# Kernel optimization log

Hardware: AMD Instinct MI355X
Metric: run time of the kernel (lower is better)

## Reference

```python
import jax, jax.numpy as jnp
import numpy as np

IMAGE_SIZE = 224
COV_HP = 1.0
SIGMA = 1.0
STEPS = 2
CUTOFF = 20.0
IMP_LO, IMP_HI = 0.5, 2.0
REL_W = 0.5
EPS = 1e-6

# Projection matrices for front/top/left views (buffer Js in the module)
JS = jnp.array([[[1, 0, 0], [0, 1, 0]],
                [[1, 0, 0], [0, 0, 1]],
                [[0, 0, 1], [0, 1, 0]]], dtype=jnp.float32)


def _blur(d, sigma):
    # d: [B,H,W]; separable Gaussian blur, 'same' padding
    r = max(1, int(3 * sigma))
    x = jnp.arange(-r, r + 1, dtype=jnp.float32)
    k = jnp.exp(-(x * x) / (2.0 * sigma * sigma))
    k = k / k.sum()
    d4 = d[:, None]  # [B,1,H,W]
    kh = k.reshape(1, 1, -1, 1)
    kw = k.reshape(1, 1, 1, -1)
    d4 = jax.lax.conv_general_dilated(d4, kh, (1, 1), [(r, r), (0, 0)],
                                      dimension_numbers=('NCHW', 'OIHW', 'NCHW'))
    d4 = jax.lax.conv_general_dilated(d4, kw, (1, 1), [(0, 0), (r, r)],
                                      dimension_numbers=('NCHW', 'OIHW', 'NCHW'))
    return d4[:, 0]


def _fill_depth_map(d, sigma, steps):
    # fill_depth_map is not defined in the source; implemented as iterative
    # Gaussian-blur hole filling (empty pixels take blurred neighborhood).
    for _ in range(steps):
        b = _blur(d, sigma)
        d = jnp.where(d > 1e-6, d, b)
    return d


def _forward(position, cov3d, opacity, importance):
    B, N, _ = position.shape
    H = W = IMAGE_SIZE
    Hh, Wh = H // 2, W // 2
    yy, xx = jnp.meshgrid(jnp.arange(Hh), jnp.arange(Wh), indexing='ij')
    grid = jnp.stack([xx, yy], axis=-1).astype(jnp.float32)  # [Hh,Wh,2]
    imp = jnp.clip(jnp.broadcast_to(importance[:, :N], (B, N)), IMP_LO, IMP_HI)
    imp = imp[:, :, None, None]
    eye3 = jnp.eye(3, dtype=cov3d.dtype)
    eye2 = jnp.eye(2, dtype=cov3d.dtype)
    maps = []
    for v in range(3):  # fixed small view loop, as in the source
        J = JS[v]  # [2,3]
        # NOTE: source mutates cov3d across the view loop; replicate that
        cov3d = (cov3d + jnp.swapaxes(cov3d, -1, -2)) * 0.5
        cov3d = cov3d + EPS * eye3
        nrm = jnp.linalg.norm(cov3d, axis=(-1, -2), keepdims=True)
        cov3d = cov3d / (nrm + EPS) * COV_HP
        cinv = jnp.linalg.inv(cov3d)                               # [B,N,3,3]
        cov2d_inv = jnp.einsum('ij,bnjk,lk->bnil', J, cinv, J)     # J C^-1 J^T
        cov2d_inv = cov2d_inv + eye2 * (EPS * 1e-4)
        proj = jnp.einsum('bnk,jk->bnj', position, J)              # [B,N,2]
        mn = proj.min(axis=1, keepdims=True)
        mx = proj.max(axis=1, keepdims=True)
        rng = mx - mn + 1e-6
        mn = mn - 0.5 * rng
        mx = mx + 0.5 * rng
        rng = mx - mn + 1e-6
        xy = jnp.clip((proj - mn) / rng * (Wh - 1), 0.0, Wh - 1)
        delta = grid[None, None] - xy[:, :, None, None, :]         # [B,N,Hh,Wh,2]
        mask_h = jnp.linalg.norm(delta, axis=-1) < CUTOFF
        mask = jnp.repeat(jnp.repeat(mask_h, 2, axis=2), 2, axis=3)
        exph = -jnp.einsum('bnhwj,bnjk,bnhwk->bnhw', delta, cov2d_inv, delta)
        exp_full = jax.image.resize(exph, (B, N, H, W), method='bilinear')
        exp_full = jnp.clip(exp_full, -20.0, 0.0)
        w = opacity[:, :, None, None] * imp * jnp.exp(exp_full)
        w = jnp.where(mask, w, 0.0)
        wmin = w.min(axis=1, keepdims=True)
        wmax = w.max(axis=1, keepdims=True)
        nw = (w - wmin) / (wmax - wmin + EPS) * REL_W + w / (w.sum(axis=1, keepdims=True) + EPS)
        dm = nw.sum(axis=1)  # [B,H,W]
        maps.append(_fill_depth_map(dm, SIGMA, STEPS))
    d = jnp.stack(maps, axis=1)  # [B,3,H,W], already 224x224 so resize is a no-op
    d = (d - d.mean()) / (jnp.std(d, ddof=1) + EPS)
    return d


def setup_inputs() -> dict:
    key = jax.random.key(0)
    k1, k2, k3 = jax.random.split(key, 3)
    B, N, MAXG = 1, 512, 1000
    return {
        'position': jax.random.normal(k1, (B, N, 3), dtype=jnp.float32),
        'cov3d': jax.random.normal(k2, (B, N, 3, 3), dtype=jnp.float32),
        'opacity': jax.random.uniform(k3, (B, N), dtype=jnp.float32),
        'importance': jnp.ones((1, MAXG), dtype=jnp.float32),
    }


def reference(position, cov3d, opacity, importance):
    return _forward(position, cov3d, opacity, importance)
```

## Files before the change

kernel.cpp:

```cpp
#include <hip/hip_runtime.h>
#include <math.h>


#define NBLOCKS 588u
#define NARR 32
#define FLAG_IDX (NARR * 32)
#define KSPLIT 4
#define QOFF 12544
#define MNOFF 602112
#define MXOFF 1204224

__device__ __forceinline__ float g_ld(const float* p) {
    return __hip_atomic_load(p, __ATOMIC_RELAXED, __HIP_MEMORY_SCOPE_AGENT);
}
__device__ __forceinline__ void g_st(float* p, float v) {
    __hip_atomic_store(p, v, __ATOMIC_RELAXED, __HIP_MEMORY_SCOPE_AGENT);
}

__device__ __forceinline__ void grid_barrier(unsigned* cnts, int arrIdx, bool poller) {
    __syncthreads();
    if (threadIdx.x == 0) {
        asm volatile("s_waitcnt vmcnt(0)" ::: "memory");
        __hip_atomic_fetch_add(&cnts[arrIdx * 32], 1u,
                               __ATOMIC_RELAXED, __HIP_MEMORY_SCOPE_AGENT);
        unsigned* flagp = &cnts[FLAG_IDX];
        if (poller) {
            for (;;) {
                unsigned s = 0;
                #pragma unroll
                for (int i = 0; i < NARR; ++i)
                    s += __hip_atomic_load(&cnts[i * 32],
                                           __ATOMIC_RELAXED, __HIP_MEMORY_SCOPE_AGENT);
                if (s == NBLOCKS) break;
                __builtin_amdgcn_s_sleep(2);
            }
            asm volatile("" ::: "memory");
            __hip_atomic_store(flagp, 1u, __ATOMIC_RELAXED, __HIP_MEMORY_SCOPE_AGENT);
        } else {
            while (__hip_atomic_load(flagp, __ATOMIC_RELAXED,
                                     __HIP_MEMORY_SCOPE_AGENT) == 0u)
                __builtin_amdgcn_s_sleep(2);
        }
    }
    __syncthreads();
}

__device__ __forceinline__ float wave_min(float v) {
    #pragma unroll
    for (int o = 32; o >= 1; o >>= 1) v = fminf(v, __shfl_xor(v, o));
    return v;
}

__global__ __launch_bounds__(512) void setup_kernel(
    const float* __restrict__ position, const float* __restrict__ cov3d,
    const float* __restrict__ opacity, const float* __restrict__ importance,
    float4* __restrict__ abc, float2* __restrict__ gxy,
    unsigned* __restrict__ cnts) {
    __shared__ float red[8 * 6];
    const int v = blockIdx.x;
    const int tid = threadIdx.x;
    const int lane = tid & 63, wave = tid >> 6;

    if (v == 0) {
        for (int i = tid; i <= FLAG_IDX; i += 512) cnts[i] = 0;
    }

    const int n = tid;
    const float p0 = position[n * 3 + 0];
    const float p1 = position[n * 3 + 1];
    const float p2 = position[n * 3 + 2];
    const float opimp = opacity[n] * fminf(fmaxf(importance[n], 0.5f), 2.0f);

    {
        float vals[6] = {p0, -p0, p1, -p1, p2, -p2};
        #pragma unroll
        for (int k = 0; k < 6; ++k) {
            float r = wave_min(vals[k]);
            if (lane == 0) red[wave * 6 + k] = r;
        }
    }
    __syncthreads();
    float mn6[6];
    #pragma unroll
    for (int k = 0; k < 6; ++k) {
        float r = red[k];
        #pragma unroll
        for (int w = 1; w < 8; ++w) r = fminf(r, red[w * 6 + k]);
        mn6[k] = r;
    }
    const float pmn[3] = {mn6[0], mn6[2], mn6[4]};
    const float pmx[3] = {-mn6[1], -mn6[3], -mn6[5]};

    float c00 = cov3d[n * 9 + 0], c01 = cov3d[n * 9 + 1], c02 = cov3d[n * 9 + 2];
    float c10 = cov3d[n * 9 + 3], c11 = cov3d[n * 9 + 4], c12 = cov3d[n * 9 + 5];
    float c20 = cov3d[n * 9 + 6], c21 = cov3d[n * 9 + 7], c22 = cov3d[n * 9 + 8];
    for (int vv = 0; vv <= v; ++vv) {
        float s01 = 0.5f * (c01 + c10);
        float s02 = 0.5f * (c02 + c20);
        float s12 = 0.5f * (c12 + c21);
        float s00 = c00 + 1e-6f;
        float s11 = c11 + 1e-6f;
        float s22 = c22 + 1e-6f;
        float nrm = sqrtf(s00 * s00 + s11 * s11 + s22 * s22 +
                          2.0f * (s01 * s01 + s02 * s02 + s12 * s12));
        float inv = 1.0f / (nrm + 1e-6f);
        c00 = s00 * inv; c11 = s11 * inv; c22 = s22 * inv;
        c01 = s01 * inv; c10 = c01; c02 = s02 * inv; c20 = c02;
        c12 = s12 * inv; c21 = c12;
    }
    float cof00 = c11 * c22 - c12 * c12;
    float cof01 = c02 * c12 - c01 * c22;
    float cof02 = c01 * c12 - c02 * c11;
    float det = c00 * cof00 + c01 * cof01 + c02 * cof02;
    float idet = 1.0f / det;
    float i00 = cof00 * idet;
    float i01 = cof01 * idet;
    float i02 = cof02 * idet;
    float i11 = (c00 * c22 - c02 * c02) * idet;
    float i12 = (c02 * c01 - c00 * c12) * idet;
    float i22 = (c00 * c11 - c01 * c01) * idet;

    float Aa, Ab, Ac, prx, pry;
    int ix, iy;
    if (v == 0)      { Aa = i00; Ab = i01; Ac = i11; prx = p0; pry = p1; ix = 0; iy = 1; }
    else if (v == 1) { Aa = i00; Ab = i02; Ac = i22; prx = p0; pry = p2; ix = 0; iy = 2; }
    else             { Aa = i22; Ab = i12; Ac = i11; prx = p2; pry = p1; ix = 2; iy = 1; }
    Aa += 1e-10f;
    Ac += 1e-10f;

    float mnx = pmn[ix], mxx = pmx[ix], mny = pmn[iy], mxy = pmx[iy];
    float rngx = mxx - mnx + 1e-6f;
    float mnx2 = mnx - 0.5f * rngx;
    float mxx2 = mxx + 0.5f * rngx;
    rngx = mxx2 - mnx2 + 1e-6f;
    float rngy = mxy - mny + 1e-6f;
    float mny2 = mny - 0.5f * rngy;
    float mxy2 = mxy + 0.5f * rngy;
    rngy = mxy2 - mny2 + 1e-6f;
    float gx = fminf(fmaxf((prx - mnx2) / rngx * 111.0f, 0.0f), 111.0f);
    float gy = fminf(fmaxf((pry - mny2) / rngy * 111.0f, 0.0f), 111.0f);

    abc[v * 512 + n] = make_float4(Aa, 2.0f * Ab, Ac, opimp);
    gxy[v * 512 + n] = make_float2(gx, gy);
}

__global__ __launch_bounds__(512) void splat_part_kernel(
    const float4* __restrict__ abc, const float2* __restrict__ gxy,
    float* __restrict__ part) {
    __shared__ float4 lsA[512];
    __shared__ float2 lsB[512];
    __shared__ int wcnt[8];
    __shared__ float4 pS[7][64], pMn[7][64], pMx[7][64];
    const int v  = blockIdx.z >> 2;
    const int kk = blockIdx.z & 3;
    const int tx0 = blockIdx.x * 16, ty0 = blockIdx.y * 16;
    const int tid = threadIdx.x;
    const int lane = tid & 63, wave = tid >> 6;

    const float4 a4 = abc[v * 512 + tid];
    const float2 g2 = gxy[v * 512 + tid];

    unsigned long long m;
    bool pass;
    {
        const float bx0 = (float)(tx0 >> 1), bx1 = (float)((tx0 + 15) >> 1);
        const float by0 = (float)(ty0 >> 1), by1 = (float)((ty0 + 15) >> 1);
        float dx = fmaxf(fmaxf(bx0 - g2.x, g2.x - bx1), 0.0f);
        float dy = fmaxf(fmaxf(by0 - g2.y, g2.y - by1), 0.0f);
        pass = (dx * dx + dy * dy) < 400.01f;
        m = __ballot(pass);
        if (lane == 0) wcnt[wave] = __popcll(m);
    }
    __syncthreads();
    int base = 0, lentot = 0;
    #pragma unroll
    for (int w = 0; w < 8; ++w) {
        int c = wcnt[w];
        if (w < wave) base += c;
        lentot += c;
    }
    if (pass) {
        int slot = base + __popcll(m & ((1ull << lane) - 1ull));
        lsA[slot] = a4;
        lsB[slot] = g2;
    }
    __syncthreads();
    const int len = lentot;

    const int qx = lane & 7, qy = lane >> 3;
    const int xh = (tx0 >> 1) + qx;
    const int yh = (ty0 >> 1) + qy;

    const int npad = (len + 63) & ~63;
    if (tid < npad - len) {
        lsA[len + tid] = make_float4(1.0f, 0.0f, 1.0f, 0.0f);
        lsB[len + tid] = make_float2(1e9f, 1e9f);
    }
    __syncthreads();

    float exA[2], eyA[2], VxA[2], VyA[2];
    #pragma unroll
    for (int p = 0; p < 2; ++p) {
        int xlo = xh - 1 + p; int xhi = min(xlo + 1, 111); xlo = max(xlo, 0);
        float wlo = p ? 0.75f : 0.25f, whi = 1.0f - wlo;
        exA[p] = wlo * (float)xlo + whi * (float)xhi;
        VxA[p] = wlo * whi * (float)(xhi - xlo) * (float)(xhi - xlo);
        int ylo = yh - 1 + p; int yhi2 = min(ylo + 1, 111); ylo = max(ylo, 0);
        eyA[p] = wlo * (float)ylo + whi * (float)yhi2;
        VyA[p] = wlo * whi * (float)(yhi2 - ylo) * (float)(yhi2 - ylo);
    }
    const float fxh = (float)xh, fyh = (float)yh;

    const int chunk = npad >> 5;
    const int cbeg = ((kk << 3) + wave) * chunk, cend = cbeg + chunk;

    float S00 = 0.f, S01 = 0.f, S10 = 0.f, S11 = 0.f;
    float mn00 = INFINITY, mn01 = INFINITY, mn10 = INFINITY, mn11 = INFINITY;
    float mx00 = -INFINITY, mx01 = -INFINITY, mx10 = -INFINITY, mx11 = -INFINITY;

    for (int i = cbeg; i < cend; i += 2) {
        float4 gA0 = lsA[i], gA1 = lsA[i + 1];
        float2 gB0 = lsB[i], gB1 = lsB[i + 1];
        #pragma unroll
        for (int u = 0; u < 2; ++u) {
            const float4 gA = u ? gA1 : gA0;
            const float2 gB = u ? gB1 : gB0;
            const float a = gA.x, b2 = gA.y, c = gA.z, op = gA.w;
            const float xx = gB.x, yy = gB.y;
            const float dxh = fxh - xx, dyh = fyh - yy;
            const bool inside = dxh * dxh + dyh * dyh < 400.0f;
            const float dx0 = exA[0] - xx, dx1 = exA[1] - xx;
            const float dy0 = eyA[0] - yy, dy1 = eyA[1] - yy;
            const float adx0 = a * dx0, adx1 = a * dx1;
            const float bdy0 = b2 * dy0, bdy1 = b2 * dy1;
            const float cdy0 = c * dy0 * dy0, cdy1 = c * dy1 * dy1;
            const float ax0 = a * VxA[0], ax1 = a * VxA[1];
            const float cy0 = c * VyA[0], cy1 = c * VyA[1];
            #pragma unroll
            for (int py = 0; py < 2; ++py) {
                const float bdyp = py ? bdy1 : bdy0;
                const float cdyp = py ? cdy1 : cdy0;
                const float cyp  = py ? cy1 : cy0;
                #pragma unroll
                for (int px = 0; px < 2; ++px) {
                    const float dxp  = px ? dx1 : dx0;
                    const float adxp = px ? adx1 : adx0;
                    const float axp  = px ? ax1 : ax0;
                    float q = dxp * (adxp + bdyp) + cdyp;
                    float bil = -((q + axp) + cyp);
                    bil = fminf(fmaxf(bil, -20.0f), 0.0f);
                    bil = inside ? bil : -1e9f;
                    float w = op * __expf(bil);
                    if (py == 0 && px == 0) { S00 += w; mn00 = fminf(mn00, w); mx00 = fmaxf(mx00, w); }
                    if (py == 0 && px == 1) { S01 += w; mn01 = fminf(mn01, w); mx01 = fmaxf(mx01, w); }
                    if (py == 1 && px == 0) { S10 += w; mn10 = fminf(mn10, w); mx10 = fmaxf(mx10, w); }
                    if (py == 1 && px == 1) { S11 += w; mn11 = fminf(mn11, w); mx11 = fmaxf(mx11, w); }
                }
            }
        }
    }
    if (wave > 0) {
        pS[wave - 1][lane]  = make_float4(S00, S01, S10, S11);
        pMn[wave - 1][lane] = make_float4(mn00, mn01, mn10, mn11);
        pMx[wave - 1][lane] = make_float4(mx00, mx01, mx10, mx11);
    }
    __syncthreads();
    if (wave == 0) {
        #pragma unroll
        for (int w = 0; w < 7; ++w) {
            float4 s = pS[w][lane], mnw = pMn[w][lane], mxw = pMx[w][lane];
            S00 += s.x; S01 += s.y; S10 += s.z; S11 += s.w;
            mn00 = fminf(mn00, mnw.x); mn01 = fminf(mn01, mnw.y);
            mn10 = fminf(mn10, mnw.z); mn11 = fminf(mn11, mnw.w);
            mx00 = fmaxf(mx00, mxw.x); mx01 = fmaxf(mx01, mxw.y);
            mx10 = fmaxf(mx10, mxw.z); mx11 = fmaxf(mx11, mxw.w);
        }
        if (len < 512) {
            mn00 = fminf(mn00, 0.f); mn01 = fminf(mn01, 0.f);
            mn10 = fminf(mn10, 0.f); mn11 = fminf(mn11, 0.f);
            mx00 = fmaxf(mx00, 0.f); mx01 = fmaxf(mx01, 0.f);
            mx10 = fmaxf(mx10, 0.f); mx11 = fmaxf(mx11, 0.f);
        }
        const int qidx = (kk * 3 + v) * QOFF + yh * 112 + xh;
        ((float4*)(part))[qidx]          = make_float4(S00, S01, S10, S11);
        ((float4*)(part + MNOFF))[qidx]  = make_float4(mn00, mn01, mn10, mn11);
        ((float4*)(part + MXOFF))[qidx]  = make_float4(mx00, mx01, mx10, mx11);
    }
}

__global__ __launch_bounds__(256, 3) void blur_norm_kernel(
    const float* __restrict__ part, float* __restrict__ out,
    float2* __restrict__ partials, unsigned* __restrict__ cnts) {
    __shared__ float A[28 * 29];
    __shared__ float T[28 * 29];
    __shared__ float r1[4], r2[4];
    __shared__ double s1[256], s2[256];
    const int v = blockIdx.z;
    const int tx0 = blockIdx.x * 16, ty0 = blockIdx.y * 16;
    const int tid = threadIdx.x;
    const int lane = tid & 63, wave = tid >> 6;
    const int bid = (v * 14 + blockIdx.y) * 14 + blockIdx.x;
    const float kw[7] = {0.00443305f, 0.05400558f, 0.24203623f, 0.39905030f,
                         0.24203623f, 0.05400558f, 0.00443305f};

    for (int idx = tid; idx < 28 * 28; idx += 256) {
        int rr = idx / 28, c = idx % 28;
        int gyy = ty0 - 6 + rr, gxx = tx0 - 6 + c;
        float val = 0.0f;
        if (gyy >= 0 && gyy < 224 && gxx >= 0 && gxx < 224) {
            const int qb = (gyy >> 1) * 112 + (gxx >> 1);
            const int comp = ((gyy & 1) << 1) | (gxx & 1);
            float S = 0.0f, mn = INFINITY, mx = -INFINITY;
            #pragma unroll
            for (int k = 0; k < KSPLIT; ++k) {
                const int fi = ((k * 3 + v) * QOFF + qb) * 4 + comp;
                S += part[fi];
                mn = fminf(mn, part[MNOFF + fi]);
                mx = fmaxf(mx, part[MXOFF + fi]);
            }
            val = 0.5f * (S - 512.0f * mn) / (mx - mn + 1e-6f) + S / (S + 1e-6f);
        }
        A[rr * 29 + c] = val;
    }
    __syncthreads();
    for (int idx = tid; idx < 22 * 28; idx += 256) {
        int rr = 3 + idx / 28, c = idx % 28;
        float s = 0.0f;
        #pragma unroll
        for (int i = 0; i < 7; ++i) s += kw[i] * A[(rr - 3 + i) * 29 + c];
        T[rr * 29 + c] = s;
    }
    __syncthreads();
    for (int idx = tid; idx < 22 * 22; idx += 256) {
        int rr = 3 + idx / 22, c = 3 + idx % 22;
        int gyy = ty0 - 6 + rr, gxx = tx0 - 6 + c;
        float s = 0.0f;
        #pragma unroll
        for (int j = 0; j < 7; ++j) s += kw[j] * T[rr * 29 + c - 3 + j];
        float ctr = A[rr * 29 + c];
        float d1 = ctr > 1e-6f ? ctr : s;
        if (gyy < 0 || gyy > 223 || gxx < 0 || gxx > 223) d1 = 0.0f;
        A[rr * 29 + c] = d1;
    }
    __syncthreads();
    for (int idx = tid; idx < 16 * 22; idx += 256) {
        int rr = 6 + idx / 22, c = 3 + idx % 22;
        float s = 0.0f;
        #pragma unroll
        for (int i = 0; i < 7; ++i) s += kw[i] * A[(rr - 3 + i) * 29 + c];
        T[rr * 29 + c] = s;
    }
    __syncthreads();
    const int rr2 = 6 + (tid >> 4), cc2 = 6 + (tid & 15);
    float d2;
    {
        float s = 0.0f;
        #pragma unroll
        for (int j = 0; j < 7; ++j) s += kw[j] * T[rr2 * 29 + cc2 - 3 + j];
        float ctr = A[rr2 * 29 + cc2];
        d2 = ctr > 1e-6f ? ctr : s;
    }
    float ls1 = d2, ls2 = d2 * d2;
    #pragma unroll
    for (int o = 32; o >= 1; o >>= 1) {
        ls1 += __shfl_xor(ls1, o);
        ls2 += __shfl_xor(ls2, o);
    }
    if (lane == 0) { r1[wave] = ls1; r2[wave] = ls2; }
    __syncthreads();
    if (tid == 0) {
        float a = r1[0] + r1[1] + r1[2] + r1[3];
        float b = r2[0] + r2[1] + r2[2] + r2[3];
        float* pb = (float*)&partials[bid];
        g_st(pb + 0, a);
        g_st(pb + 1, b);
    }

    grid_barrier(cnts, bid & (NARR - 1), bid == 0);

    double a = 0.0, b = 0.0;
    const float* pb = (const float*)partials;
    for (int i = tid; i < 588; i += 256) {
        a += (double)g_ld(pb + 2 * i);
        b += (double)g_ld(pb + 2 * i + 1);
    }
    s1[tid] = a; s2[tid] = b;
    __syncthreads();
    for (int s = 128; s >= 1; s >>= 1) {
        if (tid < s) { s1[tid] += s1[tid + s]; s2[tid] += s2[tid + s]; }
        __syncthreads();
    }
    const double M = 150528.0;
    double mean = s1[0] / M;
    double var = (s2[0] - M * mean * mean) / (M - 1.0);
    double sd = sqrt(var > 0.0 ? var : 0.0);
    const float fmean = (float)mean;
    const float finv = 1.0f / ((float)sd + 1e-6f);
    out[(v * 224 + ty0 + (tid >> 4)) * 224 + tx0 + (tid & 15)] =
        (d2 - fmean) * finv;
}

extern "C" void kernel_launch(void* const* d_in, const int* in_sizes, int n_in,
                              void* d_out, int out_size, void* d_ws, size_t ws_size,
                              hipStream_t stream) {
    const float* position   = (const float*)d_in[0];
    const float* cov3d      = (const float*)d_in[1];
    const float* opacity    = (const float*)d_in[2];
    const float* importance = (const float*)d_in[3];
    float* out = (float*)d_out;

    float* part      = (float*)d_ws;
    float2* partials = (float2*)((float*)d_ws + 1806336);
    unsigned* cnts   = (unsigned*)((float*)d_ws + 1806336 + 1176);
    float4* abc      = (float4*)((float*)d_ws + 1808640);
    float2* gxy      = (float2*)((float*)d_ws + 1808640 + 6144);

    hipLaunchKernelGGL(setup_kernel, dim3(3), dim3(512), 0, stream,
                       position, cov3d, opacity, importance, abc, gxy, cnts);
    hipLaunchKernelGGL(splat_part_kernel, dim3(14, 14, 3 * KSPLIT), dim3(512), 0,
                       stream, abc, gxy, part);
    hipLaunchKernelGGL(blur_norm_kernel, dim3(14, 14, 3), dim3(256), 0, stream,
                       part, out, partials, cnts);
}
```

Before: 97.02 us.

## Halve splat K-split, vectorize quad loads, and centralize final stats reduction

```diff
diff --git a/kernel.cpp b/kernel.cpp
--- a/kernel.cpp
+++ b/kernel.cpp
@@ -5,44 +5,17 @@
 #define NBLOCKS 588u
 #define NARR 32
 #define FLAG_IDX (NARR * 32)
-#define KSPLIT 4
+#define STAT_IDX (FLAG_IDX + 32)
+#define KSPLIT 2
 #define QOFF 12544
-#define MNOFF 602112
-#define MXOFF 1204224
+#define MNOFF 301056
+#define MXOFF 602112
 
 __device__ __forceinline__ float g_ld(const float* p) {
     return __hip_atomic_load(p, __ATOMIC_RELAXED, __HIP_MEMORY_SCOPE_AGENT);
 }
 __device__ __forceinline__ void g_st(float* p, float v) {
     __hip_atomic_store(p, v, __ATOMIC_RELAXED, __HIP_MEMORY_SCOPE_AGENT);
-}
-
-__device__ __forceinline__ void grid_barrier(unsigned* cnts, int arrIdx, bool poller) {
-    __syncthreads();
-    if (threadIdx.x == 0) {
-        asm volatile("s_waitcnt vmcnt(0)" ::: "memory");
-        __hip_atomic_fetch_add(&cnts[arrIdx * 32], 1u,
-                               __ATOMIC_RELAXED, __HIP_MEMORY_SCOPE_AGENT);
-        unsigned* flagp = &cnts[FLAG_IDX];
-        if (poller) {
-            for (;;) {
-                unsigned s = 0;
-                #pragma unroll
-                for (int i = 0; i < NARR; ++i)
-                    s += __hip_atomic_load(&cnts[i * 32],
-                                           __ATOMIC_RELAXED, __HIP_MEMORY_SCOPE_AGENT);
-                if (s == NBLOCKS) break;
-                __builtin_amdgcn_s_sleep(2);
-            }
-            asm volatile("" ::: "memory");
-            __hip_atomic_store(flagp, 1u, __ATOMIC_RELAXED, __HIP_MEMORY_SCOPE_AGENT);
-        } else {
-            while (__hip_atomic_load(flagp, __ATOMIC_RELAXED,
-                                     __HIP_MEMORY_SCOPE_AGENT) == 0u)
-                __builtin_amdgcn_s_sleep(2);
-        }
-    }
-    __syncthreads();
 }
 
 __device__ __forceinline__ float wave_min(float v) {
@@ -62,7 +35,7 @@
     const int lane = tid & 63, wave = tid >> 6;
 
     if (v == 0) {
-        for (int i = tid; i <= FLAG_IDX; i += 512) cnts[i] = 0;
+        for (int i = tid; i < STAT_IDX + 32; i += 512) cnts[i] = 0;
     }
 
     const int n = tid;
@@ -151,8 +124,8 @@
     __shared__ float2 lsB[512];
     __shared__ int wcnt[8];
     __shared__ float4 pS[7][64], pMn[7][64], pMx[7][64];
-    const int v  = blockIdx.z >> 2;
-    const int kk = blockIdx.z & 3;
+    const int v  = blockIdx.z >> 1;
+    const int kk = blockIdx.z & 1;
     const int tx0 = blockIdx.x * 16, ty0 = blockIdx.y * 16;
     const int tid = threadIdx.x;
     const int lane = tid & 63, wave = tid >> 6;
@@ -211,7 +184,7 @@
     }
     const float fxh = (float)xh, fyh = (float)yh;
 
-    const int chunk = npad >> 5;
+    const int chunk = npad >> 4;
     const int cbeg = ((kk << 3) + wave) * chunk, cend = cbeg + chunk;
 
     float S00 = 0.f, S01 = 0.f, S10 = 0.f, S11 = 0.f;
@@ -295,6 +268,7 @@
     __shared__ float T[28 * 29];
     __shared__ float r1[4], r2[4];
     __shared__ double s1[256], s2[256];
+    __shared__ float statLds[2];
     const int v = blockIdx.z;
     const int tx0 = blockIdx.x * 16, ty0 = blockIdx.y * 16;
     const int tid = threadIdx.x;
@@ -303,24 +277,37 @@
     const float kw[7] = {0.00443305f, 0.05400558f, 0.24203623f, 0.39905030f,
                          0.24203623f, 0.05400558f, 0.00443305f};
 
-    for (int idx = tid; idx < 28 * 28; idx += 256) {
-        int rr = idx / 28, c = idx % 28;
-        int gyy = ty0 - 6 + rr, gxx = tx0 - 6 + c;
-        float val = 0.0f;
-        if (gyy >= 0 && gyy < 224 && gxx >= 0 && gxx < 224) {
-            const int qb = (gyy >> 1) * 112 + (gxx >> 1);
-            const int comp = ((gyy & 1) << 1) | (gxx & 1);
-            float S = 0.0f, mn = INFINITY, mx = -INFINITY;
+    {
+        const float4* Sp  = (const float4*)part;
+        const float4* Mnp = (const float4*)(part + MNOFF);
+        const float4* Mxp = (const float4*)(part + MXOFF);
+        const int qy0 = (ty0 - 6) >> 1, qx0 = (tx0 - 6) >> 1;
+        if (tid < 196) {
+            const int qr = tid / 14, qc = tid % 14;
+            const int qgy = qy0 + qr, qgx = qx0 + qc;
+            float dmv[4] = {0.0f, 0.0f, 0.0f, 0.0f};
+            if (qgy >= 0 && qgy < 112 && qgx >= 0 && qgx < 112) {
+                const int qb = qgy * 112 + qgx;
+                const float4 S0 = Sp[(0 * 3 + v) * QOFF + qb];
+                const float4 S1 = Sp[(1 * 3 + v) * QOFF + qb];
+                const float4 n0 = Mnp[(0 * 3 + v) * QOFF + qb];
+                const float4 n1 = Mnp[(1 * 3 + v) * QOFF + qb];
+                const float4 x0 = Mxp[(0 * 3 + v) * QOFF + qb];
+                const float4 x1 = Mxp[(1 * 3 + v) * QOFF + qb];
+                const float Sc[4]  = {S0.x + S1.x, S0.y + S1.y, S0.z + S1.z, S0.w + S1.w};
+                const float mnc[4] = {fminf(n0.x, n1.x), fminf(n0.y, n1.y),
+                                      fminf(n0.z, n1.z), fminf(n0.w, n1.w)};
+                const float mxc[4] = {fmaxf(x0.x, x1.x), fmaxf(x0.y, x1.y),
+                                      fmaxf(x0.z, x1.z), fmaxf(x0.w, x1.w)};
+                #pragma unroll
+                for (int cc = 0; cc < 4; ++cc)
+                    dmv[cc] = 0.5f * (Sc[cc] - 512.0f * mnc[cc]) / (mxc[cc] - mnc[cc] + 1e-6f)
+                            + Sc[cc] / (Sc[cc] + 1e-6f);
+            }
             #pragma unroll
-            for (int k = 0; k < KSPLIT; ++k) {
-                const int fi = ((k * 3 + v) * QOFF + qb) * 4 + comp;
-                S += part[fi];
-                mn = fminf(mn, part[MNOFF + fi]);
-                mx = fmaxf(mx, part[MXOFF + fi]);
-            }
-            val = 0.5f * (S - 512.0f * mn) / (mx - mn + 1e-6f) + S / (S + 1e-6f);
-        }
-        A[rr * 29 + c] = val;
+            for (int cc = 0; cc < 4; ++cc)
+                A[(2 * qr + (cc >> 1)) * 29 + 2 * qc + (cc & 1)] = dmv[cc];
+        }
     }
     __syncthreads();
     for (int idx = tid; idx < 22 * 28; idx += 256) {
@@ -368,34 +355,72 @@
     }
     if (lane == 0) { r1[wave] = ls1; r2[wave] = ls2; }
     __syncthreads();
+
     if (tid == 0) {
         float a = r1[0] + r1[1] + r1[2] + r1[3];
         float b = r2[0] + r2[1] + r2[2] + r2[3];
         float* pb = (float*)&partials[bid];
         g_st(pb + 0, a);
         g_st(pb + 1, b);
-    }
-
-    grid_barrier(cnts, bid & (NARR - 1), bid == 0);
-
-    double a = 0.0, b = 0.0;
-    const float* pb = (const float*)partials;
-    for (int i = tid; i < 588; i += 256) {
-        a += (double)g_ld(pb + 2 * i);
-        b += (double)g_ld(pb + 2 * i + 1);
-    }
-    s1[tid] = a; s2[tid] = b;
-    __syncthreads();
-    for (int s = 128; s >= 1; s >>= 1) {
-        if (tid < s) { s1[tid] += s1[tid + s]; s2[tid] += s2[tid + s]; }
+        asm volatile("s_waitcnt vmcnt(0)" ::: "memory");
+        __hip_atomic_fetch_add(&cnts[(bid & (NARR - 1)) * 32], 1u,
+                               __ATOMIC_RELAXED, __HIP_MEMORY_SCOPE_AGENT);
+    }
+
+    float fmean, finv;
+    if (bid == 0) {
+        if (tid == 0) {
+            for (;;) {
+                unsigned s = 0;
+                #pragma unroll
+                for (int i = 0; i < NARR; ++i)
+                    s += __hip_atomic_load(&cnts[i * 32],
+                                           __ATOMIC_RELAXED, __HIP_MEMORY_SCOPE_AGENT);
+                if (s == NBLOCKS) break;
+                __builtin_amdgcn_s_sleep(2);
+            }
+        }
         __syncthreads();
-    }
-    const double M = 150528.0;
-    double mean = s1[0] / M;
-    double var = (s2[0] - M * mean * mean) / (M - 1.0);
-    double sd = sqrt(var > 0.0 ? var : 0.0);
-    const float fmean = (float)mean;
-    const float finv = 1.0f / ((float)sd + 1e-6f);
+        double a = 0.0, b = 0.0;
+        const float* pb = (const float*)partials;
+        for (int i = tid; i < 588; i += 256) {
+            a += (double)g_ld(pb + 2 * i);
+            b += (double)g_ld(pb + 2 * i + 1);
+        }
+        s1[tid] = a; s2[tid] = b;
+        __syncthreads();
+        for (int s = 128; s >= 1; s >>= 1) {
+            if (tid < s) { s1[tid] += s1[tid + s]; s2[tid] += s2[tid + s]; }
+            __syncthreads();
+        }
+        const double M = 150528.0;
+        double mean = s1[0] / M;
+        double var = (s2[0] - M * mean * mean) / (M - 1.0);
+        double sd = sqrt(var > 0.0 ? var : 0.0);
+        fmean = (float)mean;
+        finv = 1.0f / ((float)sd + 1e-6f);
+        if (tid == 0) {
+            float* st = (float*)&cnts[STAT_IDX];
+            g_st(st + 0, fmean);
+            g_st(st + 1, finv);
+            asm volatile("s_waitcnt vmcnt(0)" ::: "memory");
+            __hip_atomic_store(&cnts[FLAG_IDX], 1u,
+                               __ATOMIC_RELAXED, __HIP_MEMORY_SCOPE_AGENT);
+        }
+    } else {
+        if (tid == 0) {
+            while (__hip_atomic_load(&cnts[FLAG_IDX], __ATOMIC_RELAXED,
+                                     __HIP_MEMORY_SCOPE_AGENT) == 0u)
+                __builtin_amdgcn_s_sleep(2);
+            const float* st = (const float*)&cnts[STAT_IDX];
+            statLds[0] = g_ld(st + 0);
+            statLds[1] = g_ld(st + 1);
+        }
+        __syncthreads();
+        fmean = statLds[0];
+        finv = statLds[1];
+    }
+
     out[(v * 224 + ty0 + (tid >> 4)) * 224 + tx0 + (tid & 15)] =
         (d2 - fmean) * finv;
 }
@@ -410,10 +435,10 @@
     float* out = (float*)d_out;
 
     float* part      = (float*)d_ws;
-    float2* partials = (float2*)((float*)d_ws + 1806336);
-    unsigned* cnts   = (unsigned*)((float*)d_ws + 1806336 + 1176);
-    float4* abc      = (float4*)((float*)d_ws + 1808640);
-    float2* gxy      = (float2*)((float*)d_ws + 1808640 + 6144);
+    float2* partials = (float2*)((float*)d_ws + 903168);
+    unsigned* cnts   = (unsigned*)((float*)d_ws + 903168 + 1176);
+    float4* abc      = (float4*)((float*)d_ws + 905440);
+    float2* gxy      = (float2*)((float*)d_ws + 905440 + 6144);
 
     hipLaunchKernelGGL(setup_kernel, dim3(3), dim3(512), 0, stream,
                        position, cov3d, opacity, importance, abc, gxy, cnts);
```

After: 93.40 us. -3.7%, faster.
